# Kernel tuning notes

Measured on AMD Instinct MI355X. Metric: run time of the kernel, lower is better.

The kernel has to match this reference:

```python
import jax, jax.numpy as jnp
import numpy as np

# Production-scale dims
B, S, D = 8, 2048, 1024          # batch, seq_len, d_model
E, ES, V = 32, 128, 1024         # n_experts, expert_size, v_dim (= d_model)
K = 4                            # top-k experts per token (n_heads)


def setup_inputs() -> dict:
    key = jax.random.key(0)
    k1, k2, k3, k4 = jax.random.split(key, 4)
    return {
        "x": jax.random.normal(k1, (B, S, D), jnp.float32),
        "keys": jax.random.normal(k2, (E, D, ES), jnp.float32) * (D ** -0.5),
        "values": jax.random.normal(k3, (E, ES, V), jnp.float32) * (ES ** -0.5),
        "expert_sel": jax.random.normal(k4, (E, D), jnp.float32) * (D ** -0.5),
    }


def reference(x, keys, values, expert_sel):
    """SigmaMoELayer forward (eval mode, sigmoid selection, no bias/dropout).
    Returns (out [B,S,V], reg_loss scalar)."""
    n_experts = expert_sel.shape[0]
    # Router logits: [B, S, E]
    sel_raw = jnp.einsum('bsd,ed->bse', x, expert_sel)

    # Entropy regularization: log_softmax over experts, log-mean over all tokens
    l = jax.nn.log_softmax(sel_raw.reshape(-1, n_experts), axis=-1)   # [T, E]
    lm = jax.scipy.special.logsumexp(l, axis=0) - jnp.log(jnp.asarray(l.shape[0], l.dtype))
    reg_loss = jnp.sum(lm * jnp.exp(lm))  # == -entropy_l(lm).mean()

    # Sigmoid gating + top-k expert selection
    sel = jax.nn.sigmoid(sel_raw)
    sel_val, sel_idx = jax.lax.top_k(sel, K)                          # [B,S,K]

    # Scatter gate values onto the expert axis: gate[b,s,e] = sel_val if e selected else 0
    gate = jnp.einsum('bske,bsk->bse',
                      jax.nn.one_hot(sel_idx, n_experts, dtype=x.dtype), sel_val)

    # Expert up-projection + ReLU, gated (relu(mask*z) == mask*relu(z), experts distinct)
    h = jax.nn.relu(jnp.einsum('bsd,edf->bsef', x, keys)) * gate[..., None]  # [B,S,E,ES]
    # Expert down-projection + combine across experts
    out = jnp.einsum('bsef,efv->bsv', h, values)                      # [B,S,V]
    return out, reg_loss
```

## Files before the change

### kernel.cpp

```cpp
#include <hip/hip_runtime.h>

typedef unsigned int uint;
typedef unsigned short ushort;

#define TT 16384
#define DD 1024
#define EE 32
#define ESS 128
#define VV 1024
#define KK 4
#define TILE 64
#define NTILE_MAX 1056

typedef __attribute__((ext_vector_type(8))) short bf16x8;
typedef __attribute__((ext_vector_type(16))) float f32x16;

#define WS_SELRAW   0
#define WS_GATES    524288
#define WS_PGATE    589824
#define WS_STATS    655360
#define WS_LMSUMS   655360
#define WS_COUNTS   655392
#define WS_OFFSETS  655424
#define WS_CURSORS  655457
#define WS_NTILES   655489
#define WS_TMAPE    655490
#define WS_TMAPT    656546
#define WS_IDXS     657602
#define WS_PERM     723138
#define WS_XB       788736
#define WS_KF       9177344
#define WS_VF       11274496
#define WS_ISLOT    13371648
#define WS_STG      13437184
#define WS_NEED_U   46991616ull

__device__ __forceinline__ ushort f2b(float f) {
    uint u = __builtin_bit_cast(uint, f);
    u = (u + 0x7fffu + ((u >> 16) & 1u)) >> 16;
    return (ushort)u;
}
__device__ __forceinline__ uint bpack(float lo, float hi) {
    return (uint)f2b(lo) | ((uint)f2b(hi) << 16);
}
__device__ __forceinline__ float b2f(ushort b) {
    uint u = (uint)b << 16;
    return __builtin_bit_cast(float, u);
}

__device__ __forceinline__ void gload_lds16(const void* g, void* l) {
    __builtin_amdgcn_global_load_lds(
        (const __attribute__((address_space(1))) uint*)g,
        (__attribute__((address_space(3))) uint*)l, 16, 0, 0);
}

__global__ __launch_bounds__(256) void k_prep_k(const float* __restrict__ keys,
                                                ushort* __restrict__ kfb) {
    const int e = blockIdx.x >> 6, ks = blockIdx.x & 63;
    const int nf = threadIdx.x >> 6, l = threadIdx.x & 63;
    const int f = nf * 32 + (l & 31);
    const int d0 = ks * 16 + (l >> 5) * 8;
    const float* src = keys + ((size_t)e * DD + d0) * ESS + f;
    float v[8];
#pragma unroll
    for (int j = 0; j < 8; j++) v[j] = src[(size_t)j * ESS];
    uint4 r = { bpack(v[0], v[1]), bpack(v[2], v[3]), bpack(v[4], v[5]), bpack(v[6], v[7]) };
    const size_t off = (((size_t)e * 64 + ks) * 4 + nf) * 512 + l * 8;
    *(uint4*)(kfb + off) = r;
}

__global__ __launch_bounds__(512) void k_prep_v(const float* __restrict__ values,
                                                ushort* __restrict__ vfb) {
    const int e = blockIdx.x >> 5, nv = blockIdx.x & 31;
    const int ks = threadIdx.x >> 6, l = threadIdx.x & 63;
    const int v0 = nv * 32 + (l & 31);
    const int f0 = ks * 16 + (l >> 5) * 8;
    const float* src = values + ((size_t)e * ESS + f0) * VV + v0;
    float v[8];
#pragma unroll
    for (int j = 0; j < 8; j++) v[j] = src[(size_t)j * VV];
    uint4 r = { bpack(v[0], v[1]), bpack(v[2], v[3]), bpack(v[4], v[5]), bpack(v[6], v[7]) };
    const size_t off = (((size_t)e * 32 + nv) * 8 + ks) * 512 + l * 8;
    *(uint4*)(vfb + off) = r;
}

__global__ __launch_bounds__(256) void k_router(const float* __restrict__ x,
                                                const float* __restrict__ sel,
                                                float* __restrict__ sel_part,
                                                uint* __restrict__ xbu) {
    __shared__ float xs[64][68];
    __shared__ float ss[32][68];
    const int tid = threadIdx.x;
    const int t0 = blockIdx.x * 64;
    const int dch = blockIdx.y;
    const int el = tid & 31;
    const int tg = tid >> 5;
    float acc[8];
#pragma unroll
    for (int i = 0; i < 8; i++) acc[i] = 0.f;

    for (int dc = dch * 256; dc < dch * 256 + 256; dc += 64) {
#pragma unroll
        for (int i = 0; i < 4; i++) {
            int q = tid + 256 * i;
            int r = q >> 4, c4 = q & 15;
            size_t gi = (size_t)(t0 + r) * DD + dc + c4 * 4;
            float4 v = *(const float4*)&x[gi];
            *(float4*)&xs[r][c4 * 4] = v;
            uint2 bv = { bpack(v.x, v.y), bpack(v.z, v.w) };
            *(uint2*)&xbu[gi / 2] = bv;
        }
#pragma unroll
        for (int i = 0; i < 2; i++) {
            int q = tid + 256 * i;
            int e = q >> 4, c4 = q & 15;
            float4 v = *(const float4*)&sel[(size_t)e * DD + dc + c4 * 4];
            *(float4*)&ss[e][c4 * 4] = v;
        }
        __syncthreads();
#pragma unroll
        for (int d4 = 0; d4 < 16; d4++) {
            float4 sv = *(const float4*)&ss[el][d4 * 4];
#pragma unroll
            for (int i = 0; i < 8; i++) {
                float4 xv = *(const float4*)&xs[tg * 8 + i][d4 * 4];
                acc[i] += xv.x * sv.x + xv.y * sv.y + xv.z * sv.z + xv.w * sv.w;
            }
        }
        __syncthreads();
    }
    float* dst = sel_part + (size_t)dch * TT * EE;
#pragma unroll
    for (int i = 0; i < 8; i++)
        dst[(size_t)(t0 + tg * 8 + i) * EE + el] = acc[i];
}

__global__ __launch_bounds__(256) void k_token(const float* __restrict__ sel_part,
                                               float* __restrict__ gates,
                                               int* __restrict__ idxs,
                                               float* __restrict__ lm_sums,
                                               int* __restrict__ counts) {
    __shared__ int hist[EE];
    __shared__ float lmh[EE];
    const int tid = threadIdx.x;
    if (tid < EE) { hist[tid] = 0; lmh[tid] = 0.f; }
    __syncthreads();

    const int t = blockIdx.x * 256 + tid;
    float v[32];
#pragma unroll
    for (int j = 0; j < 8; j++) {
        float4 q0 = *(const float4*)&sel_part[(size_t)t * EE + j * 4];
        float4 q1 = *(const float4*)&sel_part[((size_t)TT + t) * EE + j * 4];
        float4 q2 = *(const float4*)&sel_part[((size_t)2 * TT + t) * EE + j * 4];
        float4 q3 = *(const float4*)&sel_part[((size_t)3 * TT + t) * EE + j * 4];
        v[j * 4 + 0] = ((q0.x + q1.x) + (q2.x + q3.x));
        v[j * 4 + 1] = ((q0.y + q1.y) + (q2.y + q3.y));
        v[j * 4 + 2] = ((q0.z + q1.z) + (q2.z + q3.z));
        v[j * 4 + 3] = ((q0.w + q1.w) + (q2.w + q3.w));
    }
    float m = v[0];
#pragma unroll
    for (int e = 1; e < 32; e++) m = fmaxf(m, v[e]);
    float s = 0.f;
#pragma unroll
    for (int e = 0; e < 32; e++) s += expf(v[e] - m);
    const float lse = logf(s) + m;

    float sg[32];
#pragma unroll
    for (int e = 0; e < 32; e++) sg[e] = 1.f / (1.f + expf(-v[e]));

    unsigned taken = 0u;
#pragma unroll
    for (int k = 0; k < KK; k++) {
        float best = -1.f; int bi = 0;
#pragma unroll
        for (int e = 0; e < 32; e++) {
            bool free_e = !((taken >> e) & 1u);
            if (free_e && sg[e] > best) { best = sg[e]; bi = e; }
        }
        taken |= 1u << bi;
        gates[t * KK + k] = best;
        idxs[t * KK + k] = bi;
        atomicAdd(&hist[bi], 1);
    }

#pragma unroll
    for (int e = 0; e < 32; e++) {
        float pv = expf(v[e] - lse);
#pragma unroll
        for (int o = 32; o >= 1; o >>= 1) pv += __shfl_xor(pv, o, 64);
        if ((tid & 63) == 0) atomicAdd(&lmh[e], pv);
    }
    __syncthreads();
    if (tid < EE) {
        atomicAdd(&counts[tid], hist[tid]);
        atomicAdd(&lm_sums[tid], lmh[tid]);
    }
}

__global__ void k_scan(const int* __restrict__ counts, int* __restrict__ offsets,
                       int* __restrict__ cursors, int* __restrict__ tmape,
                       int* __restrict__ tmapt, int* __restrict__ ntiles,
                       const float* __restrict__ lm_sums, float* __restrict__ out_reg) {
    const int lane = threadIdx.x;
    int c = (lane < EE) ? counts[lane] : 0;
    int p = c;
#pragma unroll
    for (int o = 1; o < 32; o <<= 1) { int u = __shfl_up(p, o, 64); if (lane >= o) p += u; }
    const int off = p - c;
    if (lane < EE) { offsets[lane] = off; cursors[lane] = off; }
    if (lane == EE - 1) offsets[EE] = p;

    int nt = (c + TILE - 1) / TILE;
    int q = nt;
#pragma unroll
    for (int o = 1; o < 32; o <<= 1) { int u = __shfl_up(q, o, 64); if (lane >= o) q += u; }
    const int tb = q - nt;
    if (lane < EE)
        for (int j = 0; j < nt; j++) { tmape[tb + j] = lane; tmapt[tb + j] = j; }
    if (lane == EE - 1) ntiles[0] = q;

    float rv = 0.f;
    if (lane < EE) {
        float pe = lm_sums[lane] * (1.f / (float)TT);
        rv = pe * logf(pe);
    }
#pragma unroll
    for (int o = 16; o >= 1; o >>= 1) rv += __shfl_down(rv, o, 64);
    if (lane == 0) out_reg[0] = rv;
}

__global__ __launch_bounds__(256) void k_scatter(const int* __restrict__ idxs,
                                                 const float* __restrict__ gates,
                                                 int* __restrict__ cursors,
                                                 int* __restrict__ perm,
                                                 float* __restrict__ pgate,
                                                 int* __restrict__ islot) {
    __shared__ int lh[EE];
    __shared__ int lbase[EE];
    const int tid = threadIdx.x;
    if (tid < EE) lh[tid] = 0;
    __syncthreads();
    const int t = blockIdx.x * 256 + tid;
    int ee[KK], rk[KK];
#pragma unroll
    for (int k = 0; k < KK; k++) {
        ee[k] = idxs[t * KK + k];
        rk[k] = atomicAdd(&lh[ee[k]], 1);
    }
    __syncthreads();
    if (tid < EE) lbase[tid] = atomicAdd(&cursors[tid], lh[tid]);
    __syncthreads();
#pragma unroll
    for (int k = 0; k < KK; k++) {
        int pos = lbase[ee[k]] + rk[k];
        perm[pos] = t;
        pgate[pos] = gates[t * KK + k];
        islot[t * KK + k] = pos;
    }
}

template <bool STG>
__global__ __launch_bounds__(256, 2) void k_expert(
    const ushort* __restrict__ xb, const ushort* __restrict__ kfb,
    const ushort* __restrict__ vfb,
    const int* __restrict__ perm, const float* __restrict__ pgate,
    const int* __restrict__ offsets, const int* __restrict__ counts,
    const int* __restrict__ tmape, const int* __restrict__ tmapt,
    const int* __restrict__ ntiles, ushort* __restrict__ stg,
    float* __restrict__ out)
{
    __shared__ __align__(1024) char xsb[64 * 512];
    __shared__ __align__(16) ushort hs[64][128];
    __shared__ float gl[64];
    __shared__ int tl[64];

    const int bid = (blockIdx.x & 7) * 132 + (blockIdx.x >> 3);
    if (bid >= ntiles[0]) return;
    const int e = tmape[bid];
    const int base = offsets[e] + tmapt[bid] * TILE;
    const int nr = min(TILE, offsets[e] + counts[e] - base);
    const int tid = threadIdx.x;

    if (tid < 64) {
        int tok = 0; float g = 0.f;
        if (tid < nr) { tok = perm[base + tid]; g = pgate[base + tid]; }
        tl[tid] = tok; gl[tid] = g;
    }
    __syncthreads();

    const int lane = tid & 63, wid = tid >> 6;
    const int wm = wid >> 1, wn = wid & 1;
    const int l31 = lane & 31, l5 = lane >> 5;

    const char* xbytes = (const char*)xb;
    const ushort* kb = kfb + ((size_t)e * 256 + wn * 2) * 512 + lane * 8;

    int srow[8]; const char* ssrc[8];
#pragma unroll
    for (int i = 0; i < 8; i++) {
        int ldsb = (wid * 8 + i) * 1024;
        int lb = ldsb + lane * 16;
        int row = lb >> 9;
        int colb = lb & 511;
        srow[i] = ldsb;
        ssrc[i] = xbytes + (size_t)tl[row] * 2048 + (colb ^ ((row & 31) << 4));
    }

    f32x16 acc0, acc1;
#pragma unroll
    for (int r = 0; r < 16; r++) { acc0[r] = 0.f; acc1[r] = 0.f; }

    bf16x8 b0p[8], b1p[8];
#pragma unroll
    for (int j = 0; j < 8; j++) {
        b0p[j] = *(const bf16x8*)(kb + (size_t)j * 2048);
        b1p[j] = *(const bf16x8*)(kb + (size_t)j * 2048 + 512);
    }

    const int aRrow = wm * 32 + l31;
    for (int c = 0; c < 4; c++) {
#pragma unroll
        for (int i = 0; i < 8; i++)
            gload_lds16(ssrc[i] + c * 512, xsb + srow[i]);
        __syncthreads();

#pragma unroll
        for (int ksl = 0; ksl < 16; ksl++) {
            bf16x8 a = *(const bf16x8*)(xsb + aRrow * 512 +
                                        ((ksl * 32 + l5 * 16) ^ (l31 << 4)));
            int ks = c * 16 + ksl;
            acc0 = __builtin_amdgcn_mfma_f32_32x32x16_bf16(a, b0p[ksl & 7], acc0, 0, 0, 0);
            acc1 = __builtin_amdgcn_mfma_f32_32x32x16_bf16(a, b1p[ksl & 7], acc1, 0, 0, 0);
            int nk = (ks + 8) & 63;
            b0p[ksl & 7] = *(const bf16x8*)(kb + (size_t)nk * 2048);
            b1p[ksl & 7] = *(const bf16x8*)(kb + (size_t)nk * 2048 + 512);
        }
        __syncthreads();
    }

#pragma unroll
    for (int r = 0; r < 16; r++) {
        int row = (r & 3) + 8 * (r >> 2) + 4 * l5;
        int grow = wm * 32 + row;
        float g = gl[grow];
        int c0 = wn * 64 + l31;
        int c1 = c0 + 32;
        int sw = (grow & 7) << 3;
        hs[grow][c0 ^ sw] = f2b(fmaxf(acc0[r], 0.f) * g);
        hs[grow][c1 ^ sw] = f2b(fmaxf(acc1[r], 0.f) * g);
    }
    __syncthreads();

    bf16x8 af[8];
    const int hr = wm * 32 + l31;
    const int hsw = (hr & 7) << 3;
#pragma unroll
    for (int ks = 0; ks < 8; ks++) {
        int cc = ks * 16 + l5 * 8;
        af[ks] = *(const bf16x8*)&hs[hr][cc ^ hsw];
    }

    int ptok[16]; int prow[16]; bool pv[16];
#pragma unroll
    for (int r = 0; r < 16; r++) {
        int row = wm * 32 + (r & 3) + 8 * (r >> 2) + 4 * l5;
        prow[r] = row; ptok[r] = tl[row]; pv[r] = (row < nr);
    }

    const ushort* vb = vfb + ((size_t)e * 32 + wn * 16) * 4096 + lane * 8;
    bf16x8 vp[2][8];
#pragma unroll
    for (int ks = 0; ks < 8; ks++) {
        vp[0][ks] = *(const bf16x8*)(vb + (size_t)ks * 512);
        vp[1][ks] = *(const bf16x8*)(vb + (size_t)(8 + ks) * 512);
    }

#pragma unroll
    for (int nv = 0; nv < 16; nv++) {
        f32x16 acc;
#pragma unroll
        for (int r = 0; r < 16; r++) acc[r] = 0.f;
#pragma unroll
        for (int ks = 0; ks < 8; ks++)
            acc = __builtin_amdgcn_mfma_f32_32x32x16_bf16(af[ks], vp[nv & 1][ks], acc, 0, 0, 0);
        if (nv + 2 < 16) {
#pragma unroll
            for (int ks = 0; ks < 8; ks++)
                vp[nv & 1][ks] = *(const bf16x8*)(vb + ((size_t)(nv + 2) * 8 + ks) * 512);
        }
        const int colb = wn * 512 + nv * 32 + l31;
#pragma unroll
        for (int r = 0; r < 16; r++) {
            if (!pv[r]) continue;
            if (STG)
                stg[(size_t)(base + prow[r]) * VV + colb] = f2b(acc[r]);
            else
                atomicAdd(&out[(size_t)ptok[r] * VV + colb], acc[r]);
        }
    }
}

__global__ __launch_bounds__(256) void k_combine(const ushort* __restrict__ stg,
                                                 const int* __restrict__ islot,
                                                 float* __restrict__ out) {
    const int tid = threadIdx.x;
    const int t = blockIdx.x * 2 + (tid >> 7);
    const int c8 = (tid & 127) * 8;
    const int4 sl = *(const int4*)&islot[t * KK];
    float acc[8];
#pragma unroll
    for (int j = 0; j < 8; j++) acc[j] = 0.f;
    const int slots[4] = { sl.x, sl.y, sl.z, sl.w };
#pragma unroll
    for (int k = 0; k < KK; k++) {
        bf16x8 v = *(const bf16x8*)(stg + (size_t)slots[k] * VV + c8);
#pragma unroll
        for (int j = 0; j < 8; j++) acc[j] += b2f((ushort)v[j]);
    }
    float4 o0 = { acc[0], acc[1], acc[2], acc[3] };
    float4 o1 = { acc[4], acc[5], acc[6], acc[7] };
    *(float4*)&out[(size_t)t * VV + c8] = o0;
    *(float4*)&out[(size_t)t * VV + c8 + 4] = o1;
}

extern "C" void kernel_launch(void* const* d_in, const int* in_sizes, int n_in,
                              void* d_out, int out_size, void* d_ws, size_t ws_size,
                              hipStream_t stream) {
    const float* x      = (const float*)d_in[0];
    const float* keys   = (const float*)d_in[1];
    const float* values = (const float*)d_in[2];
    const float* esel   = (const float*)d_in[3];
    float* out = (float*)d_out;

    float* wsf = (float*)d_ws;
    int*   wsi = (int*)d_ws;

    float* gates   = wsf + WS_GATES;
    float* pgate   = wsf + WS_PGATE;
    float* lm_sums = wsf + WS_LMSUMS;
    int*   counts  = wsi + WS_COUNTS;
    int*   offsets = wsi + WS_OFFSETS;
    int*   cursors = wsi + WS_CURSORS;
    int*   ntiles  = wsi + WS_NTILES;
    int*   tmape   = wsi + WS_TMAPE;
    int*   tmapt   = wsi + WS_TMAPT;
    int*   idxs    = wsi + WS_IDXS;
    int*   perm    = wsi + WS_PERM;
    int*   islot   = wsi + WS_ISLOT;
    uint*   xbu = (uint*)(wsf + WS_XB);
    ushort* xb  = (ushort*)xbu;
    ushort* kfb = (ushort*)(wsf + WS_KF);
    ushort* vfb = (ushort*)(wsf + WS_VF);
    ushort* stg = (ushort*)(wsf + WS_STG);

    const bool use_stg = ws_size >= WS_NEED_U * 4ull;
    float* sel_part = use_stg ? (float*)stg : (float*)kfb;

    if (!use_stg)
        hipMemsetAsync(d_out, 0, (size_t)TT * VV * sizeof(float), stream);
    hipMemsetAsync(wsf + WS_STATS, 0, 64 * sizeof(float), stream);

    k_router<<<dim3(TT / 64, 4), 256, 0, stream>>>(x, esel, sel_part, xbu);
    k_token<<<TT / 256, 256, 0, stream>>>(sel_part, gates, idxs, lm_sums, counts);

    k_prep_k<<<EE * 64, 256, 0, stream>>>(keys, kfb);
    k_prep_v<<<EE * 32, 512, 0, stream>>>(values, vfb);

    k_scan<<<1, 64, 0, stream>>>(counts, offsets, cursors, tmape, tmapt, ntiles,
                                 lm_sums, out + (size_t)TT * VV);
    k_scatter<<<TT / 256, 256, 0, stream>>>(idxs, gates, cursors, perm, pgate, islot);
    if (use_stg) {
        k_expert<true><<<NTILE_MAX, 256, 0, stream>>>(xb, kfb, vfb, perm, pgate,
                                                      offsets, counts, tmape, tmapt,
                                                      ntiles, stg, out);
        k_combine<<<TT / 2, 256, 0, stream>>>(stg, islot, out);
    } else {
        k_expert<false><<<NTILE_MAX, 256, 0, stream>>>(xb, kfb, vfb, perm, pgate,
                                                       offsets, counts, tmape, tmapt,
                                                       ntiles, stg, out);
    }
}
```

Baseline: 219.3 us.

## Double-buffer expert X tiles, cut registers for 3 waves/SIMD, split router D further

New measurement: 214.0 us. 1.02x faster.

```diff
diff --git a/kernel.cpp b/kernel.cpp
--- a/kernel.cpp
+++ b/kernel.cpp
@@ -11,6 +11,7 @@
 #define KK 4
 #define TILE 64
 #define NTILE_MAX 1056
+#define RSPLIT 8
 
 typedef __attribute__((ext_vector_type(8))) short bf16x8;
 typedef __attribute__((ext_vector_type(16))) float f32x16;
@@ -99,7 +100,8 @@
 #pragma unroll
     for (int i = 0; i < 8; i++) acc[i] = 0.f;
 
-    for (int dc = dch * 256; dc < dch * 256 + 256; dc += 64) {
+    const int dlen = DD / RSPLIT;
+    for (int dc = dch * dlen; dc < dch * dlen + dlen; dc += 64) {
 #pragma unroll
         for (int i = 0; i < 4; i++) {
             int q = tid + 256 * i;
@@ -150,14 +152,14 @@
     float v[32];
 #pragma unroll
     for (int j = 0; j < 8; j++) {
-        float4 q0 = *(const float4*)&sel_part[(size_t)t * EE + j * 4];
-        float4 q1 = *(const float4*)&sel_part[((size_t)TT + t) * EE + j * 4];
-        float4 q2 = *(const float4*)&sel_part[((size_t)2 * TT + t) * EE + j * 4];
-        float4 q3 = *(const float4*)&sel_part[((size_t)3 * TT + t) * EE + j * 4];
-        v[j * 4 + 0] = ((q0.x + q1.x) + (q2.x + q3.x));
-        v[j * 4 + 1] = ((q0.y + q1.y) + (q2.y + q3.y));
-        v[j * 4 + 2] = ((q0.z + q1.z) + (q2.z + q3.z));
-        v[j * 4 + 3] = ((q0.w + q1.w) + (q2.w + q3.w));
+        float4 q[RSPLIT];
+#pragma unroll
+        for (int p = 0; p < RSPLIT; p++)
+            q[p] = *(const float4*)&sel_part[((size_t)p * TT + t) * EE + j * 4];
+        v[j * 4 + 0] = ((q[0].x + q[1].x) + (q[2].x + q[3].x)) + ((q[4].x + q[5].x) + (q[6].x + q[7].x));
+        v[j * 4 + 1] = ((q[0].y + q[1].y) + (q[2].y + q[3].y)) + ((q[4].y + q[5].y) + (q[6].y + q[7].y));
+        v[j * 4 + 2] = ((q[0].z + q[1].z) + (q[2].z + q[3].z)) + ((q[4].z + q[5].z) + (q[6].z + q[7].z));
+        v[j * 4 + 3] = ((q[0].w + q[1].w) + (q[2].w + q[3].w)) + ((q[4].w + q[5].w) + (q[6].w + q[7].w));
     }
     float m = v[0];
 #pragma unroll
@@ -263,7 +265,7 @@
 }
 
 template <bool STG>
-__global__ __launch_bounds__(256, 2) void k_expert(
+__global__ __launch_bounds__(256, 3) void k_expert(
     const ushort* __restrict__ xb, const ushort* __restrict__ kfb,
     const ushort* __restrict__ vfb,
     const int* __restrict__ perm, const float* __restrict__ pgate,
@@ -272,7 +274,7 @@
     const int* __restrict__ ntiles, ushort* __restrict__ stg,
     float* __restrict__ out)
 {
-    __shared__ __align__(1024) char xsb[64 * 512];
+    __shared__ __align__(1024) char xsb[2][64 * 256];
     __shared__ __align__(16) ushort hs[64][128];
     __shared__ float gl[64];
     __shared__ int tl[64];
@@ -298,45 +300,51 @@
     const char* xbytes = (const char*)xb;
     const ushort* kb = kfb + ((size_t)e * 256 + wn * 2) * 512 + lane * 8;
 
-    int srow[8]; const char* ssrc[8];
-#pragma unroll
-    for (int i = 0; i < 8; i++) {
-        int ldsb = (wid * 8 + i) * 1024;
-        int lb = ldsb + lane * 16;
-        int row = lb >> 9;
-        int colb = lb & 511;
-        srow[i] = ldsb;
-        ssrc[i] = xbytes + (size_t)tl[row] * 2048 + (colb ^ ((row & 31) << 4));
+    int srow[4]; const char* ssrc[4];
+#pragma unroll
+    for (int i = 0; i < 4; i++) {
+        srow[i] = wid * 4096 + i * 1024;
+        int row = wid * 16 + i * 4 + (lane >> 4);
+        int colb = (lane & 15) * 16;
+        ssrc[i] = xbytes + (size_t)tl[row] * 2048 + (colb ^ ((row & 15) << 4));
     }
 
     f32x16 acc0, acc1;
 #pragma unroll
     for (int r = 0; r < 16; r++) { acc0[r] = 0.f; acc1[r] = 0.f; }
 
-    bf16x8 b0p[8], b1p[8];
-#pragma unroll
-    for (int j = 0; j < 8; j++) {
+    bf16x8 b0p[4], b1p[4];
+#pragma unroll
+    for (int j = 0; j < 4; j++) {
         b0p[j] = *(const bf16x8*)(kb + (size_t)j * 2048);
         b1p[j] = *(const bf16x8*)(kb + (size_t)j * 2048 + 512);
     }
 
-    const int aRrow = wm * 32 + l31;
-    for (int c = 0; c < 4; c++) {
-#pragma unroll
-        for (int i = 0; i < 8; i++)
-            gload_lds16(ssrc[i] + c * 512, xsb + srow[i]);
-        __syncthreads();
-
-#pragma unroll
-        for (int ksl = 0; ksl < 16; ksl++) {
-            bf16x8 a = *(const bf16x8*)(xsb + aRrow * 512 +
-                                        ((ksl * 32 + l5 * 16) ^ (l31 << 4)));
-            int ks = c * 16 + ksl;
-            acc0 = __builtin_amdgcn_mfma_f32_32x32x16_bf16(a, b0p[ksl & 7], acc0, 0, 0, 0);
-            acc1 = __builtin_amdgcn_mfma_f32_32x32x16_bf16(a, b1p[ksl & 7], acc1, 0, 0, 0);
-            int nk = (ks + 8) & 63;
-            b0p[ksl & 7] = *(const bf16x8*)(kb + (size_t)nk * 2048);
-            b1p[ksl & 7] = *(const bf16x8*)(kb + (size_t)nk * 2048 + 512);
+    const int hr = wm * 32 + l31;
+    const int asw = (hr & 15) << 4;
+
+#pragma unroll
+    for (int i = 0; i < 4; i++)
+        gload_lds16(ssrc[i], xsb[0] + srow[i]);
+    __syncthreads();
+
+    for (int c = 0; c < 8; c++) {
+        const int cur = c & 1;
+        if (c < 7) {
+#pragma unroll
+            for (int i = 0; i < 4; i++)
+                gload_lds16(ssrc[i] + (c + 1) * 256, xsb[cur ^ 1] + srow[i]);
+        }
+        const char* xcur = xsb[cur];
+#pragma unroll
+        for (int ksl = 0; ksl < 8; ksl++) {
+            bf16x8 a = *(const bf16x8*)(xcur + hr * 256 + ((ksl * 32 + l5 * 16) ^ asw));
+            int ks = c * 8 + ksl;
+            acc0 = __builtin_amdgcn_mfma_f32_32x32x16_bf16(a, b0p[ksl & 3], acc0, 0, 0, 0);
+            acc1 = __builtin_amdgcn_mfma_f32_32x32x16_bf16(a, b1p[ksl & 3], acc1, 0, 0, 0);
+            int nk = (ks + 4) & 63;
+            b0p[ksl & 3] = *(const bf16x8*)(kb + (size_t)nk * 2048);
+            b1p[ksl & 3] = *(const bf16x8*)(kb + (size_t)nk * 2048 + 512);
         }
         __syncthreads();
     }
@@ -355,7 +363,6 @@
     __syncthreads();
 
     bf16x8 af[8];
-    const int hr = wm * 32 + l31;
     const int hsw = (hr & 7) << 3;
 #pragma unroll
     for (int ks = 0; ks < 8; ks++) {
@@ -363,19 +370,12 @@
         af[ks] = *(const bf16x8*)&hs[hr][cc ^ hsw];
     }
 
-    int ptok[16]; int prow[16]; bool pv[16];
-#pragma unroll
-    for (int r = 0; r < 16; r++) {
-        int row = wm * 32 + (r & 3) + 8 * (r >> 2) + 4 * l5;
-        prow[r] = row; ptok[r] = tl[row]; pv[r] = (row < nr);
-    }
-
     const ushort* vb = vfb + ((size_t)e * 32 + wn * 16) * 4096 + lane * 8;
-    bf16x8 vp[2][8];
-#pragma unroll
-    for (int ks = 0; ks < 8; ks++) {
-        vp[0][ks] = *(const bf16x8*)(vb + (size_t)ks * 512);
-        vp[1][ks] = *(const bf16x8*)(vb + (size_t)(8 + ks) * 512);
+    bf16x8 vpa[4], vpb[4];
+#pragma unroll
+    for (int j = 0; j < 4; j++) {
+        vpa[j] = *(const bf16x8*)(vb + (size_t)j * 512);
+        vpb[j] = *(const bf16x8*)(vb + (size_t)(4 + j) * 512);
     }
 
 #pragma unroll
@@ -384,21 +384,31 @@
 #pragma unroll
         for (int r = 0; r < 16; r++) acc[r] = 0.f;
 #pragma unroll
-        for (int ks = 0; ks < 8; ks++)
-            acc = __builtin_amdgcn_mfma_f32_32x32x16_bf16(af[ks], vp[nv & 1][ks], acc, 0, 0, 0);
-        if (nv + 2 < 16) {
-#pragma unroll
-            for (int ks = 0; ks < 8; ks++)
-                vp[nv & 1][ks] = *(const bf16x8*)(vb + ((size_t)(nv + 2) * 8 + ks) * 512);
+        for (int ks = 0; ks < 4; ks++)
+            acc = __builtin_amdgcn_mfma_f32_32x32x16_bf16(af[ks], vpa[ks], acc, 0, 0, 0);
+        if (nv < 15) {
+#pragma unroll
+            for (int j = 0; j < 4; j++)
+                vpa[j] = *(const bf16x8*)(vb + ((size_t)(nv + 1) * 8 + j) * 512);
+        }
+#pragma unroll
+        for (int ks = 0; ks < 4; ks++)
+            acc = __builtin_amdgcn_mfma_f32_32x32x16_bf16(af[4 + ks], vpb[ks], acc, 0, 0, 0);
+        if (nv < 15) {
+#pragma unroll
+            for (int j = 0; j < 4; j++)
+                vpb[j] = *(const bf16x8*)(vb + ((size_t)(nv + 1) * 8 + 4 + j) * 512);
         }
         const int colb = wn * 512 + nv * 32 + l31;
 #pragma unroll
         for (int r = 0; r < 16; r++) {
-            if (!pv[r]) continue;
-            if (STG)
-                stg[(size_t)(base + prow[r]) * VV + colb] = f2b(acc[r]);
-            else
-                atomicAdd(&out[(size_t)ptok[r] * VV + colb], acc[r]);
+            int row = wm * 32 + (r & 3) + 8 * (r >> 2) + 4 * l5;
+            if (row < nr) {
+                if (STG)
+                    stg[(size_t)(base + row) * VV + colb] = f2b(acc[r]);
+                else
+                    atomicAdd(&out[(size_t)tl[row] * VV + colb], acc[r]);
+            }
         }
     }
 }
@@ -463,7 +473,7 @@
         hipMemsetAsync(d_out, 0, (size_t)TT * VV * sizeof(float), stream);
     hipMemsetAsync(wsf + WS_STATS, 0, 64 * sizeof(float), stream);
 
-    k_router<<<dim3(TT / 64, 4), 256, 0, stream>>>(x, esel, sel_part, xbu);
+    k_router<<<dim3(TT / 64, RSPLIT), 256, 0, stream>>>(x, esel, sel_part, xbu);
     k_token<<<TT / 256, 256, 0, stream>>>(sel_part, gates, idxs, lm_sums, counts);
 
     k_prep_k<<<EE * 64, 256, 0, stream>>>(keys, kfb);
```
